# Kernel optimization log

Measured on AMD Instinct MI355X. Metric: run time of the kernel, lower is better.

Reference implementation:

```python
import jax, jax.numpy as jnp
import numpy as np

N_EXPERTS = 8
TOP_K = 2


def setup_inputs() -> dict:
    key = jax.random.key(0)
    ks = jax.random.split(key, 5)
    B, T, D, E, H = 4, 2048, 1024, N_EXPERTS, 2730  # H = int(2*D*4/3)
    x = jax.random.normal(ks[0], (B, T, D), dtype=jnp.float32)
    gate_w = jax.random.normal(ks[1], (E, D), dtype=jnp.float32) * 0.02
    w1 = jax.random.normal(ks[2], (E, H, D), dtype=jnp.float32) * 0.02
    w3 = jax.random.normal(ks[3], (E, H, D), dtype=jnp.float32) * 0.02
    w2 = jax.random.normal(ks[4], (E, D, H), dtype=jnp.float32) * 0.02
    return {"x": x, "gate_w": gate_w, "w1": w1, "w3": w3, "w2": w2}


def reference(x, gate_w, w1, w3, w2):
    B, T, D = x.shape
    E = gate_w.shape[0]
    x_flat = x.reshape(-1, D)  # [N, D], N = B*T
    N = x_flat.shape[0]

    # Router: top-k over softmax probabilities, renormalized over selected experts
    logits = x_flat @ gate_w.T                      # [N, E]
    probs = jax.nn.softmax(logits, axis=-1)         # [N, E]
    top_v, top_i = jax.lax.top_k(probs, TOP_K)      # [N, K]
    top_v = top_v / jnp.sum(top_v, axis=-1, keepdims=True)

    # Dense combine weights [N, E]: weight of expert e for each token (0 if not selected).
    # top_k indices are distinct per token, so scatter-add equals scatter-set here.
    combine = jnp.zeros((N, E), dtype=x.dtype).at[
        jnp.arange(N)[:, None], top_i
    ].add(top_v)

    # Weighted combine of SwiGLU experts (loop over small fixed expert count).
    out = jnp.zeros_like(x_flat)
    for e in range(E):
        gate = jax.nn.silu(x_flat @ w1[e].T)        # [N, H]
        up = x_flat @ w3[e].T                       # [N, H]
        y = (gate * up) @ w2[e].T                   # [N, D]
        out = out + combine[:, e:e + 1] * y

    aux_loss = jnp.asarray(0.0, dtype=x.dtype)  # use_aux_loss=False / eval mode
    return out.reshape(B, T, D), aux_loss
```

## Files before the change

### kernel.cpp

```cpp
#include <hip/hip_runtime.h>
#include <hip/hip_bf16.h>

#define N_TOK 8192
#define D_DIM 1024
#define E_NUM 8
#define H_DIM 2730
#define HP    2816
#define NP    5632
#define NROWS (N_TOK*2)
#define MAXTILES 136
#define MAXT256  72

typedef __bf16 bf16;
typedef __bf16 bf16x8 __attribute__((ext_vector_type(8)));
typedef __bf16 bf16x4 __attribute__((ext_vector_type(4)));
typedef float  f32x4  __attribute__((ext_vector_type(4)));

__device__ __forceinline__ void gload_lds16(const bf16* g, bf16* l) {
  __builtin_amdgcn_global_load_lds((const __attribute__((address_space(1))) void*)g,
                                   (__attribute__((address_space(3))) void*)l, 16, 0, 0);
}
#define VMCNT(n) asm volatile("s_waitcnt vmcnt(" #n ")" ::: "memory")
#define LGKM0()  asm volatile("s_waitcnt lgkmcnt(0)" ::: "memory")
#define BAR() __builtin_amdgcn_s_barrier()

__global__ void conv13_kernel(const float* __restrict__ w1, const float* __restrict__ w3,
                              bf16* __restrict__ Bp) {
  int i = blockIdx.x * blockDim.x + threadIdx.x;
  if (i >= E_NUM * NP * 128) return;
  int c8 = i & 127;
  int r  = (i >> 7) % NP;
  int e  = i / (NP * 128);
  int hc = ((r >> 5) << 4) + (r & 15);
  bf16x8 o;
  if (hc < H_DIM) {
    const float* s = (((r >> 4) & 1) ? w3 : w1) + ((long)e * H_DIM + hc) * D_DIM + c8 * 8;
    float4 a0 = ((const float4*)s)[0], a1 = ((const float4*)s)[1];
    o[0]=(bf16)a0.x; o[1]=(bf16)a0.y; o[2]=(bf16)a0.z; o[3]=(bf16)a0.w;
    o[4]=(bf16)a1.x; o[5]=(bf16)a1.y; o[6]=(bf16)a1.z; o[7]=(bf16)a1.w;
  } else {
    #pragma unroll
    for (int j = 0; j < 8; j++) o[j] = (bf16)0.f;
  }
  ((bf16x8*)Bp)[i] = o;
}

__global__ void conv_w2_kernel(const float* __restrict__ src, bf16* __restrict__ dst) {
  int i = blockIdx.x * blockDim.x + threadIdx.x;
  if (i >= E_NUM * D_DIM * (HP / 8)) return;
  int c8 = i % (HP / 8);
  int row = i / (HP / 8);
  int c = c8 * 8;
  const float* s = src + (long)row * H_DIM + c;
  bf16x8 o;
  #pragma unroll
  for (int j = 0; j < 8; j++) o[j] = (c + j < H_DIM) ? (bf16)s[j] : (bf16)0.f;
  ((bf16x8*)dst)[i] = o;
}

__global__ void router_kernel(const float* __restrict__ x, const float* __restrict__ gw,
                              int* __restrict__ topi, float* __restrict__ topw,
                              int* __restrict__ counts) {
  int t = blockIdx.x * (blockDim.x >> 6) + (threadIdx.x >> 6);
  int lane = threadIdx.x & 63;
  if (t >= N_TOK) return;
  const float* xr = x + (long)t * D_DIM;
  float acc[E_NUM];
  #pragma unroll
  for (int e = 0; e < E_NUM; e++) acc[e] = 0.f;
  for (int j = 0; j < D_DIM / 64; j++) {
    float xv = xr[j * 64 + lane];
    #pragma unroll
    for (int e = 0; e < E_NUM; e++) acc[e] += xv * gw[e * D_DIM + j * 64 + lane];
  }
  #pragma unroll
  for (int e = 0; e < E_NUM; e++) {
    float v = acc[e];
    #pragma unroll
    for (int s = 32; s > 0; s >>= 1) v += __shfl_xor(v, s, 64);
    acc[e] = v;
  }
  if (lane == 0) {
    int b0 = -1, b1 = -1; float v0 = -1e30f, v1 = -1e30f;
    #pragma unroll
    for (int e = 0; e < E_NUM; e++) {
      float v = acc[e];
      if (v > v0) { v1 = v0; b1 = b0; v0 = v; b0 = e; }
      else if (v > v1) { v1 = v; b1 = e; }
    }
    float w0 = 1.f / (1.f + expf(v1 - v0));
    topi[t * 2] = b0; topi[t * 2 + 1] = b1;
    topw[t * 2] = w0; topw[t * 2 + 1] = 1.f - w0;
    atomicAdd(&counts[b0], 1); atomicAdd(&counts[b1], 1);
  }
}

__global__ void tiles_kernel(const int* __restrict__ counts, int* __restrict__ offs,
                             int* __restrict__ tlist, int* __restrict__ tlist2) {
  if (threadIdx.x == 0) {
    int s = 0, idx = 0, idx2 = 0;
    for (int e = 0; e < E_NUM; e++) {
      offs[e] = s;
      int ne = counts[e];
      s += ne;
      int nt = (ne + 127) >> 7;
      for (int t = 0; t < nt; t++) tlist[idx++] = (e << 8) | t;
      int nt2 = (ne + 255) >> 8;
      for (int t = 0; t < nt2; t++) tlist2[idx2++] = (e << 8) | t;
    }
    offs[E_NUM] = s;
    for (; idx < MAXTILES; idx++) tlist[idx] = -1;
    for (; idx2 < MAXT256; idx2++) tlist2[idx2] = -1;
  }
}

__global__ void scatter_kernel(const int* __restrict__ topi, const float* __restrict__ topw,
                               const int* __restrict__ offs, int* __restrict__ cursor,
                               int* __restrict__ rowmap, float* __restrict__ roww,
                               int* __restrict__ rowoftok) {
  int i = blockIdx.x * blockDim.x + threadIdx.x;
  if (i >= NROWS) return;
  int e = topi[i];
  int pos = atomicAdd(&cursor[e], 1);
  int row = offs[e] + pos;
  rowmap[row] = i >> 1;
  roww[row] = topw[i];
  rowoftok[i] = row;
}

__global__ void gather_kernel(const float* __restrict__ x, const int* __restrict__ rowmap,
                              bf16* __restrict__ Xg) {
  int r = blockIdx.x * (blockDim.x >> 6) + (threadIdx.x >> 6);
  int lane = threadIdx.x & 63;
  if (r >= NROWS) return;
  int t = rowmap[r];
  const float4* src = (const float4*)(x + (long)t * D_DIM);
  bf16x4* dst = (bf16x4*)(Xg + (long)r * D_DIM);
  #pragma unroll
  for (int j = 0; j < 4; j++) {
    float4 v = src[j * 64 + lane];
    bf16x4 o; o[0]=(bf16)v.x; o[1]=(bf16)v.y; o[2]=(bf16)v.z; o[3]=(bf16)v.w;
    dst[j * 64 + lane] = o;
  }
}

__global__ void combine_kernel(const bf16* __restrict__ y, const int* __restrict__ rowoftok,
                               const float* __restrict__ topw, float* __restrict__ out) {
  int t = blockIdx.x * (blockDim.x >> 6) + (threadIdx.x >> 6);
  int lane = threadIdx.x & 63;
  if (t >= N_TOK) return;
  int r0 = rowoftok[t * 2], r1 = rowoftok[t * 2 + 1];
  float w0 = topw[t * 2], w1 = topw[t * 2 + 1];
  const bf16x8* y0 = (const bf16x8*)(y + (long)r0 * D_DIM);
  const bf16x8* y1 = (const bf16x8*)(y + (long)r1 * D_DIM);
  float* o = out + (long)t * D_DIM;
  #pragma unroll
  for (int j = 0; j < 2; j++) {
    bf16x8 a = y0[j * 64 + lane], b = y1[j * 64 + lane];
    float4 v0, v1;
    v0.x = w0*(float)a[0] + w1*(float)b[0]; v0.y = w0*(float)a[1] + w1*(float)b[1];
    v0.z = w0*(float)a[2] + w1*(float)b[2]; v0.w = w0*(float)a[3] + w1*(float)b[3];
    v1.x = w0*(float)a[4] + w1*(float)b[4]; v1.y = w0*(float)a[5] + w1*(float)b[5];
    v1.z = w0*(float)a[6] + w1*(float)b[6]; v1.w = w0*(float)a[7] + w1*(float)b[7];
    float4* op = (float4*)(o + (j * 64 + lane) * 8);
    op[0] = v0; op[1] = v1;
  }
}


#define G1_STAGE(T) do { int sb_ = ((T) & 3) * 8192; \
    gload_lds16(aSrc0 + (T) * 32, smem + sb_ + wv * 512); \
    gload_lds16(aSrc1 + (T) * 32, smem + sb_ + 4096 + wv * 512); \
    gload_lds16(bSrc0 + (T) * 32, smem + 32768 + sb_ + wv * 512); \
    gload_lds16(bSrc1 + (T) * 32, smem + 32768 + sb_ + 4096 + wv * 512); \
  } while (0)

#define G1_READ0(SB) do { \
    _Pragma("unroll") for (int m_ = 0; m_ < 4; m_++) \
      aF0[m_] = *(const bf16x8*)&smem[(SB) + (wr * 64 + m_ * 16 + fr) * 32 + qp]; \
    _Pragma("unroll") for (int q_ = 0; q_ < 4; q_++) \
      bF[q_] = *(const bf16x8*)&smem[32768 + (SB) + ((q_ >> 1) * 128 + wc * 32 + (q_ & 1) * 16 + fr) * 32 + qp]; \
  } while (0)

#define G1_MFMA0() do { __builtin_amdgcn_s_setprio(1); \
    _Pragma("unroll") for (int m_ = 0; m_ < 4; m_++) \
    _Pragma("unroll") for (int q_ = 0; q_ < 4; q_++) \
      acc[0][q_ >> 1][m_][q_ & 1] = __builtin_amdgcn_mfma_f32_16x16x32_bf16(aF0[m_], bF[q_], acc[0][q_ >> 1][m_][q_ & 1], 0, 0, 0); \
    __builtin_amdgcn_s_setprio(0); } while (0)

#define G1_READ1(SB) do { \
    _Pragma("unroll") for (int m_ = 0; m_ < 4; m_++) \
      aF1[m_] = *(const bf16x8*)&smem[(SB) + (128 + wr * 64 + m_ * 16 + fr) * 32 + qp]; \
  } while (0)

#define G1_MFMA1() do { __builtin_amdgcn_s_setprio(1); \
    _Pragma("unroll") for (int m_ = 0; m_ < 4; m_++) \
    _Pragma("unroll") for (int q_ = 0; q_ < 4; q_++) \
      acc[1][q_ >> 1][m_][q_ & 1] = __builtin_amdgcn_mfma_f32_16x16x32_bf16(aF1[m_], bF[q_], acc[1][q_ >> 1][m_][q_ & 1], 0, 0, 0); \
    __builtin_amdgcn_s_setprio(0); } while (0)

__global__ __launch_bounds__(512, 2) void gemm1_kernel(
    const bf16* __restrict__ Xg, const bf16* __restrict__ Bp,
    const int* __restrict__ counts, const int* __restrict__ offs,
    const int* __restrict__ tlist2, bf16* __restrict__ h) {
  int te = tlist2[blockIdx.x];
  if (te < 0) return;
  int e = te >> 8, tm = te & 255;
  int ne = counts[e];
  int row_base = offs[e];
  int n0 = blockIdx.y * 256;

  __shared__ bf16 smem[65536];
  int tid = threadIdx.x, wv = tid >> 6, lane = tid & 63;
  int wr = wv >> 2, wc = wv & 3;
  int fr = lane & 15, hi = lane >> 4;
  int qp = (hi ^ ((fr >> 1) & 3)) * 8;
  int srcq = ((lane & 3) ^ ((lane >> 3) & 3)) * 8;
  int srow = lane >> 2;

  f32x4 acc[2][2][4][2];
  #pragma unroll
  for (int a = 0; a < 2; a++)
    #pragma unroll
    for (int b = 0; b < 2; b++)
      #pragma unroll
      for (int m = 0; m < 4; m++)
        #pragma unroll
        for (int n = 0; n < 2; n++) acc[a][b][m][n] = (f32x4)0.f;

  const bf16* Bpe = Bp + (long)e * NP * D_DIM;
  int ra0 = row_base + min(tm * 256 + wv * 16 + srow, ne - 1);
  int ra1 = row_base + min(tm * 256 + 128 + wv * 16 + srow, ne - 1);
  const bf16* aSrc0 = Xg + (long)ra0 * D_DIM + srcq;
  const bf16* aSrc1 = Xg + (long)ra1 * D_DIM + srcq;
  const bf16* bSrc0 = Bpe + (long)(n0 + wv * 16 + srow) * D_DIM + srcq;
  const bf16* bSrc1 = Bpe + (long)(n0 + 128 + wv * 16 + srow) * D_DIM + srcq;

  bf16x8 aF0[4], aF1[4], bF[4];

  G1_STAGE(0); G1_STAGE(1); G1_STAGE(2);
  VMCNT(8); BAR();

  for (int t = 0; t < 29; t++) {
    int sb = (t & 3) * 8192;
    G1_READ0(sb);
    G1_STAGE(t + 3);
    BAR();
    G1_MFMA0();
    G1_READ1(sb);
    G1_MFMA1();
    LGKM0(); VMCNT(8); BAR();
  }
  { int sb = (29 & 3) * 8192; G1_READ0(sb); BAR(); G1_MFMA0(); G1_READ1(sb); G1_MFMA1(); LGKM0(); VMCNT(4); BAR(); }
  { int sb = (30 & 3) * 8192; G1_READ0(sb); BAR(); G1_MFMA0(); G1_READ1(sb); G1_MFMA1(); LGKM0(); VMCNT(0); BAR(); }
  { int sb = (31 & 3) * 8192; G1_READ0(sb); G1_MFMA0(); G1_READ1(sb); G1_MFMA1(); }

  int crow4 = hi * 4;
  #pragma unroll
  for (int mh = 0; mh < 2; mh++)
    #pragma unroll
    for (int m = 0; m < 4; m++)
      #pragma unroll
      for (int j = 0; j < 4; j++) {
        int rloc = tm * 256 + mh * 128 + wr * 64 + m * 16 + crow4 + j;
        if (rloc < ne) {
          long hrow = (long)(row_base + rloc) * HP;
          #pragma unroll
          for (int nh = 0; nh < 2; nh++) {
            int hc0 = (n0 + nh * 128 + wc * 32) >> 1;
            float g = acc[mh][nh][m][0][j], u = acc[mh][nh][m][1][j];
            h[hrow + hc0 + fr] = (bf16)((g / (1.f + __expf(-g))) * u);
          }
        }
      }
}

#define G2_STAGE(SB, T) do { \
    _Pragma("unroll") for (int L_ = 0; L_ < 2; L_++) \
      gload_lds16(aS[L_] + (T) * 32, smem2 + (SB) + w * 1024 + L_ * 512); \
    _Pragma("unroll") for (int L_ = 0; L_ < 4; L_++) \
      gload_lds16(bS[L_] + (T) * 32, smem2 + (SB) + 4096 + w * 2048 + L_ * 512); \
  } while (0)

#define G2_READ0(SB) do { \
    _Pragma("unroll") for (int m_ = 0; m_ < 4; m_++) \
      af[m_] = *(const bf16x8*)&smem2[(SB) + (wr * 64 + m_ * 16 + fr) * 32 + qp]; \
    _Pragma("unroll") for (int n_ = 0; n_ < 4; n_++) \
      bf0[n_] = *(const bf16x8*)&smem2[(SB) + 4096 + (wc * 128 + n_ * 16 + fr) * 32 + qp]; \
  } while (0)

#define G2_MFMA0() do { __builtin_amdgcn_s_setprio(1); \
    _Pragma("unroll") for (int m_ = 0; m_ < 4; m_++) \
    _Pragma("unroll") for (int n_ = 0; n_ < 4; n_++) \
      acc[m_][n_] = __builtin_amdgcn_mfma_f32_16x16x32_bf16(af[m_], bf0[n_], acc[m_][n_], 0, 0, 0); \
    __builtin_amdgcn_s_setprio(0); } while (0)

#define G2_READ1(SB) do { \
    _Pragma("unroll") for (int n_ = 0; n_ < 4; n_++) \
      bf1[n_] = *(const bf16x8*)&smem2[(SB) + 4096 + (wc * 128 + (n_ + 4) * 16 + fr) * 32 + qp]; \
  } while (0)

#define G2_MFMA1() do { __builtin_amdgcn_s_setprio(1); \
    _Pragma("unroll") for (int m_ = 0; m_ < 4; m_++) \
    _Pragma("unroll") for (int n_ = 0; n_ < 4; n_++) \
      acc[m_][n_ + 4] = __builtin_amdgcn_mfma_f32_16x16x32_bf16(af[m_], bf1[n_], acc[m_][n_ + 4], 0, 0, 0); \
    __builtin_amdgcn_s_setprio(0); } while (0)

__global__ __launch_bounds__(256, 2) void gemm2_kernel(
    const bf16* __restrict__ h, const bf16* __restrict__ w2b,
    const int* __restrict__ counts, const int* __restrict__ offs,
    const int* __restrict__ tlist, bf16* __restrict__ y) {
  int te = tlist[blockIdx.x];
  if (te < 0) return;
  int e = te >> 8, tm = te & 255;
  int ne = counts[e];
  int row_base = offs[e];
  int n0 = blockIdx.y * 256;

  __shared__ bf16 smem2[3 * 12288];
  int tid = threadIdx.x, w = tid >> 6, lane = tid & 63;
  int wr = w >> 1, wc = w & 1;
  int fr = lane & 15, hi = lane >> 4;
  int qp = (hi ^ ((fr >> 1) & 3)) * 8;
  int srcq = ((lane & 3) ^ ((lane >> 3) & 3)) * 8;
  int srow = lane >> 2;

  f32x4 acc[4][8];
  #pragma unroll
  for (int m = 0; m < 4; m++)
    #pragma unroll
    for (int n = 0; n < 8; n++) acc[m][n] = (f32x4)0.f;

  const bf16* w2e = w2b + (long)e * D_DIM * HP;
  const bf16* aS[2];
  const bf16* bS[4];
  #pragma unroll
  for (int L = 0; L < 2; L++) {
    int ra = row_base + min(tm * 128 + w * 32 + L * 16 + srow, ne - 1);
    aS[L] = h + (long)ra * HP + srcq;
  }
  #pragma unroll
  for (int L = 0; L < 4; L++) {
    int rb = n0 + w * 64 + L * 16 + srow;
    bS[L] = w2e + (long)rb * HP + srcq;
  }

  bf16x8 af[4], bf0[4], bf1[4];

  G2_STAGE(0, 0); G2_STAGE(12288, 1);
  VMCNT(6); BAR();

  int sbC = 0, sbS = 24576;
  for (int t = 0; t < 86; t++) {
    G2_READ0(sbC);
    G2_STAGE(sbS, t + 2);
    BAR();
    G2_MFMA0();
    G2_READ1(sbC);
    G2_MFMA1();
    LGKM0(); VMCNT(6); BAR();
    sbC += 12288; if (sbC > 24576) sbC = 0;
    sbS += 12288; if (sbS > 24576) sbS = 0;
  }
  { G2_READ0(sbC); BAR(); G2_MFMA0(); G2_READ1(sbC); G2_MFMA1(); LGKM0(); VMCNT(0); BAR();
    sbC += 12288; if (sbC > 24576) sbC = 0; }
  { G2_READ0(sbC); G2_MFMA0(); G2_READ1(sbC); G2_MFMA1(); }

  int crow4 = hi * 4;
  #pragma unroll
  for (int m = 0; m < 4; m++)
    #pragma unroll
    for (int j = 0; j < 4; j++) {
      int rloc = tm * 128 + wr * 64 + m * 16 + crow4 + j;
      if (rloc < ne) {
        long yrow = (long)(row_base + rloc) * D_DIM;
        #pragma unroll
        for (int n = 0; n < 8; n++) {
          int col = n0 + wc * 128 + n * 16 + fr;
          y[yrow + col] = (bf16)acc[m][n][j];
        }
      }
    }
}

extern "C" void kernel_launch(void* const* d_in, const int* in_sizes, int n_in,
                              void* d_out, int out_size, void* d_ws, size_t ws_size,
                              hipStream_t stream) {
  const float* x  = (const float*)d_in[0];
  const float* gw = (const float*)d_in[1];
  const float* w1 = (const float*)d_in[2];
  const float* w3 = (const float*)d_in[3];
  const float* w2 = (const float*)d_in[4];
  float* out = (float*)d_out;

  char* ws = (char*)d_ws;
  int*   counts   = (int*)(ws);
  int*   cursor   = (int*)(ws + 64);
  int*   offs     = (int*)(ws + 128);
  int*   tlist    = (int*)(ws + 192);
  int*   tlist2   = (int*)(ws + 768);
  int*   topi     = (int*)(ws + 2048);
  float* topw     = (float*)(ws + 2048 + 65536);
  int*   rowmap   = (int*)(ws + 2048 + 131072);
  float* roww     = (float*)(ws + 2048 + 196608);
  int*   rowoftok = (int*)(ws + 2048 + 262144);
  char*  big      = ws + 2048 + 327680;
  bf16* Bp   = (bf16*)big;
  bf16* w2b  = (bf16*)big;
  bf16* Xg   = Bp + (size_t)E_NUM * NP * D_DIM;
  bf16* hbuf = Xg + (size_t)NROWS * D_DIM;
  bf16* ybuf = Xg;

  hipMemsetAsync((char*)d_out + (size_t)(out_size - 1) * sizeof(float), 0, sizeof(float), stream);
  hipMemsetAsync(ws, 0, 256, stream);

  int nbp = E_NUM * NP * 128;
  conv13_kernel<<<(nbp + 255) / 256, 256, 0, stream>>>(w1, w3, Bp);

  router_kernel<<<N_TOK / 4, 256, 0, stream>>>(x, gw, topi, topw, counts);
  tiles_kernel<<<1, 64, 0, stream>>>(counts, offs, tlist, tlist2);
  scatter_kernel<<<(NROWS + 255) / 256, 256, 0, stream>>>(topi, topw, offs, cursor, rowmap, roww, rowoftok);
  gather_kernel<<<NROWS / 4, 256, 0, stream>>>(x, rowmap, Xg);

  dim3 g1(MAXT256, NP / 256);
  gemm1_kernel<<<g1, 512, 0, stream>>>(Xg, Bp, counts, offs, tlist2, hbuf);

  int w2n = E_NUM * D_DIM * (HP / 8);
  conv_w2_kernel<<<(w2n + 255) / 256, 256, 0, stream>>>(w2, w2b);

  dim3 g2(MAXTILES, D_DIM / 256);
  gemm2_kernel<<<g2, 256, 0, stream>>>(hbuf, w2b, counts, offs, tlist, ybuf);
  combine_kernel<<<N_TOK / 4, 256, 0, stream>>>(ybuf, rowoftok, topw, out);
}
```

Measured before the change: 758.9 us.

## Shrink GEMM1 to 128x256 tiles and GEMM2 to 128x128 tiles

GEMM1 drops its 256x256 tile and 512-thread block, 4-stage pipeline for a 128x256 tile with 256 threads and a 3-stage LDS ring, reusing the GEMM2 tile list. GEMM2 narrows its N tile from 256 to 128 and raises the occupancy hint to 3 blocks per CU. The aim is less per-expert padding waste and more blocks to fill the CUs. The cost is less operand reuse per block and more global traffic for the weight and activation reloads.

```diff
diff --git a/kernel.cpp b/kernel.cpp
--- a/kernel.cpp
+++ b/kernel.cpp
@@ -9,7 +9,6 @@
 #define NP    5632
 #define NROWS (N_TOK*2)
 #define MAXTILES 136
-#define MAXT256  72
 
 typedef __bf16 bf16;
 typedef __bf16 bf16x8 __attribute__((ext_vector_type(8)));
@@ -96,21 +95,18 @@
 }
 
 __global__ void tiles_kernel(const int* __restrict__ counts, int* __restrict__ offs,
-                             int* __restrict__ tlist, int* __restrict__ tlist2) {
+                             int* __restrict__ tlist) {
   if (threadIdx.x == 0) {
-    int s = 0, idx = 0, idx2 = 0;
+    int s = 0, idx = 0;
     for (int e = 0; e < E_NUM; e++) {
       offs[e] = s;
       int ne = counts[e];
       s += ne;
       int nt = (ne + 127) >> 7;
       for (int t = 0; t < nt; t++) tlist[idx++] = (e << 8) | t;
-      int nt2 = (ne + 255) >> 8;
-      for (int t = 0; t < nt2; t++) tlist2[idx2++] = (e << 8) | t;
     }
     offs[E_NUM] = s;
     for (; idx < MAXTILES; idx++) tlist[idx] = -1;
-    for (; idx2 < MAXT256; idx2++) tlist2[idx2] = -1;
   }
 }
 
@@ -168,145 +164,136 @@
 }
 
 
-#define G1_STAGE(T) do { int sb_ = ((T) & 3) * 8192; \
-    gload_lds16(aSrc0 + (T) * 32, smem + sb_ + wv * 512); \
-    gload_lds16(aSrc1 + (T) * 32, smem + sb_ + 4096 + wv * 512); \
-    gload_lds16(bSrc0 + (T) * 32, smem + 32768 + sb_ + wv * 512); \
-    gload_lds16(bSrc1 + (T) * 32, smem + 32768 + sb_ + 4096 + wv * 512); \
+#define G1_STAGE(SB, T) do { \
+    _Pragma("unroll") for (int L_ = 0; L_ < 2; L_++) \
+      gload_lds16(aS[L_] + (T) * 32, smem + (SB) + w * 1024 + L_ * 512); \
+    _Pragma("unroll") for (int L_ = 0; L_ < 4; L_++) \
+      gload_lds16(bS[L_] + (T) * 32, smem + (SB) + 4096 + w * 2048 + L_ * 512); \
   } while (0)
 
 #define G1_READ0(SB) do { \
     _Pragma("unroll") for (int m_ = 0; m_ < 4; m_++) \
-      aF0[m_] = *(const bf16x8*)&smem[(SB) + (wr * 64 + m_ * 16 + fr) * 32 + qp]; \
+      af[m_] = *(const bf16x8*)&smem[(SB) + (wr * 64 + m_ * 16 + fr) * 32 + qp]; \
     _Pragma("unroll") for (int q_ = 0; q_ < 4; q_++) \
-      bF[q_] = *(const bf16x8*)&smem[32768 + (SB) + ((q_ >> 1) * 128 + wc * 32 + (q_ & 1) * 16 + fr) * 32 + qp]; \
+      bf0[q_] = *(const bf16x8*)&smem[(SB) + 4096 + (wc * 128 + q_ * 16 + fr) * 32 + qp]; \
   } while (0)
 
 #define G1_MFMA0() do { __builtin_amdgcn_s_setprio(1); \
     _Pragma("unroll") for (int m_ = 0; m_ < 4; m_++) \
     _Pragma("unroll") for (int q_ = 0; q_ < 4; q_++) \
-      acc[0][q_ >> 1][m_][q_ & 1] = __builtin_amdgcn_mfma_f32_16x16x32_bf16(aF0[m_], bF[q_], acc[0][q_ >> 1][m_][q_ & 1], 0, 0, 0); \
+      acc[m_][q_] = __builtin_amdgcn_mfma_f32_16x16x32_bf16(af[m_], bf0[q_], acc[m_][q_], 0, 0, 0); \
     __builtin_amdgcn_s_setprio(0); } while (0)
 
 #define G1_READ1(SB) do { \
-    _Pragma("unroll") for (int m_ = 0; m_ < 4; m_++) \
-      aF1[m_] = *(const bf16x8*)&smem[(SB) + (128 + wr * 64 + m_ * 16 + fr) * 32 + qp]; \
+    _Pragma("unroll") for (int q_ = 0; q_ < 4; q_++) \
+      bf1[q_] = *(const bf16x8*)&smem[(SB) + 4096 + (wc * 128 + (q_ + 4) * 16 + fr) * 32 + qp]; \
   } while (0)
 
 #define G1_MFMA1() do { __builtin_amdgcn_s_setprio(1); \
     _Pragma("unroll") for (int m_ = 0; m_ < 4; m_++) \
     _Pragma("unroll") for (int q_ = 0; q_ < 4; q_++) \
-      acc[1][q_ >> 1][m_][q_ & 1] = __builtin_amdgcn_mfma_f32_16x16x32_bf16(aF1[m_], bF[q_], acc[1][q_ >> 1][m_][q_ & 1], 0, 0, 0); \
+      acc[m_][q_ + 4] = __builtin_amdgcn_mfma_f32_16x16x32_bf16(af[m_], bf1[q_], acc[m_][q_ + 4], 0, 0, 0); \
     __builtin_amdgcn_s_setprio(0); } while (0)
 
-__global__ __launch_bounds__(512, 2) void gemm1_kernel(
+__global__ __launch_bounds__(256, 2) void gemm1_kernel(
     const bf16* __restrict__ Xg, const bf16* __restrict__ Bp,
     const int* __restrict__ counts, const int* __restrict__ offs,
-    const int* __restrict__ tlist2, bf16* __restrict__ h) {
-  int te = tlist2[blockIdx.x];
+    const int* __restrict__ tlist, bf16* __restrict__ h) {
+  int te = tlist[blockIdx.x];
   if (te < 0) return;
   int e = te >> 8, tm = te & 255;
   int ne = counts[e];
   int row_base = offs[e];
   int n0 = blockIdx.y * 256;
 
-  __shared__ bf16 smem[65536];
-  int tid = threadIdx.x, wv = tid >> 6, lane = tid & 63;
-  int wr = wv >> 2, wc = wv & 3;
+  __shared__ bf16 smem[3 * 12288];
+  int tid = threadIdx.x, w = tid >> 6, lane = tid & 63;
+  int wr = w >> 1, wc = w & 1;
   int fr = lane & 15, hi = lane >> 4;
   int qp = (hi ^ ((fr >> 1) & 3)) * 8;
   int srcq = ((lane & 3) ^ ((lane >> 3) & 3)) * 8;
   int srow = lane >> 2;
 
-  f32x4 acc[2][2][4][2];
-  #pragma unroll
-  for (int a = 0; a < 2; a++)
-    #pragma unroll
-    for (int b = 0; b < 2; b++)
-      #pragma unroll
-      for (int m = 0; m < 4; m++)
-        #pragma unroll
-        for (int n = 0; n < 2; n++) acc[a][b][m][n] = (f32x4)0.f;
+  f32x4 acc[4][8];
+  #pragma unroll
+  for (int m = 0; m < 4; m++)
+    #pragma unroll
+    for (int q = 0; q < 8; q++) acc[m][q] = (f32x4)0.f;
 
   const bf16* Bpe = Bp + (long)e * NP * D_DIM;
-  int ra0 = row_base + min(tm * 256 + wv * 16 + srow, ne - 1);
-  int ra1 = row_base + min(tm * 256 + 128 + wv * 16 + srow, ne - 1);
-  const bf16* aSrc0 = Xg + (long)ra0 * D_DIM + srcq;
-  const bf16* aSrc1 = Xg + (long)ra1 * D_DIM + srcq;
-  const bf16* bSrc0 = Bpe + (long)(n0 + wv * 16 + srow) * D_DIM + srcq;
-  const bf16* bSrc1 = Bpe + (long)(n0 + 128 + wv * 16 + srow) * D_DIM + srcq;
-
-  bf16x8 aF0[4], aF1[4], bF[4];
-
-  G1_STAGE(0); G1_STAGE(1); G1_STAGE(2);
-  VMCNT(8); BAR();
-
-  for (int t = 0; t < 29; t++) {
-    int sb = (t & 3) * 8192;
-    G1_READ0(sb);
-    G1_STAGE(t + 3);
+  const bf16* aS[2];
+  const bf16* bS[4];
+  #pragma unroll
+  for (int L = 0; L < 2; L++) {
+    int ra = row_base + min(tm * 128 + w * 32 + L * 16 + srow, ne - 1);
+    aS[L] = Xg + (long)ra * D_DIM + srcq;
+  }
+  #pragma unroll
+  for (int L = 0; L < 4; L++) {
+    int rb = n0 + w * 64 + L * 16 + srow;
+    bS[L] = Bpe + (long)rb * D_DIM + srcq;
+  }
+
+  bf16x8 af[4], bf0[4], bf1[4];
+
+  G1_STAGE(0, 0); G1_STAGE(12288, 1);
+  VMCNT(6); BAR();
+
+  int sbC = 0, sbS = 24576;
+  for (int t = 0; t < 30; t++) {
+    G1_READ0(sbC);
+    G1_STAGE(sbS, t + 2);
     BAR();
     G1_MFMA0();
-    G1_READ1(sb);
+    G1_READ1(sbC);
     G1_MFMA1();
-    LGKM0(); VMCNT(8); BAR();
-  }
-  { int sb = (29 & 3) * 8192; G1_READ0(sb); BAR(); G1_MFMA0(); G1_READ1(sb); G1_MFMA1(); LGKM0(); VMCNT(4); BAR(); }
-  { int sb = (30 & 3) * 8192; G1_READ0(sb); BAR(); G1_MFMA0(); G1_READ1(sb); G1_MFMA1(); LGKM0(); VMCNT(0); BAR(); }
-  { int sb = (31 & 3) * 8192; G1_READ0(sb); G1_MFMA0(); G1_READ1(sb); G1_MFMA1(); }
+    LGKM0(); VMCNT(6); BAR();
+    sbC += 12288; if (sbC > 24576) sbC = 0;
+    sbS += 12288; if (sbS > 24576) sbS = 0;
+  }
+  { G1_READ0(sbC); BAR(); G1_MFMA0(); G1_READ1(sbC); G1_MFMA1(); LGKM0(); VMCNT(0); BAR();
+    sbC += 12288; if (sbC > 24576) sbC = 0; }
+  { G1_READ0(sbC); G1_MFMA0(); G1_READ1(sbC); G1_MFMA1(); }
 
   int crow4 = hi * 4;
   #pragma unroll
-  for (int mh = 0; mh < 2; mh++)
-    #pragma unroll
-    for (int m = 0; m < 4; m++)
-      #pragma unroll
-      for (int j = 0; j < 4; j++) {
-        int rloc = tm * 256 + mh * 128 + wr * 64 + m * 16 + crow4 + j;
-        if (rloc < ne) {
-          long hrow = (long)(row_base + rloc) * HP;
-          #pragma unroll
-          for (int nh = 0; nh < 2; nh++) {
-            int hc0 = (n0 + nh * 128 + wc * 32) >> 1;
-            float g = acc[mh][nh][m][0][j], u = acc[mh][nh][m][1][j];
-            h[hrow + hc0 + fr] = (bf16)((g / (1.f + __expf(-g))) * u);
-          }
+  for (int m = 0; m < 4; m++)
+    #pragma unroll
+    for (int j = 0; j < 4; j++) {
+      int rloc = tm * 128 + wr * 64 + m * 16 + crow4 + j;
+      if (rloc < ne) {
+        long hrow = (long)(row_base + rloc) * HP;
+        #pragma unroll
+        for (int p = 0; p < 4; p++) {
+          int col = (n0 >> 1) + wc * 64 + p * 16 + fr;
+          float g = acc[m][2 * p][j], u = acc[m][2 * p + 1][j];
+          h[hrow + col] = (bf16)((g / (1.f + __expf(-g))) * u);
         }
       }
+    }
 }
 
 #define G2_STAGE(SB, T) do { \
     _Pragma("unroll") for (int L_ = 0; L_ < 2; L_++) \
       gload_lds16(aS[L_] + (T) * 32, smem2 + (SB) + w * 1024 + L_ * 512); \
-    _Pragma("unroll") for (int L_ = 0; L_ < 4; L_++) \
-      gload_lds16(bS[L_] + (T) * 32, smem2 + (SB) + 4096 + w * 2048 + L_ * 512); \
+    _Pragma("unroll") for (int L_ = 0; L_ < 2; L_++) \
+      gload_lds16(bS[L_] + (T) * 32, smem2 + (SB) + 4096 + w * 1024 + L_ * 512); \
   } while (0)
 
-#define G2_READ0(SB) do { \
+#define G2_READ(SB) do { \
     _Pragma("unroll") for (int m_ = 0; m_ < 4; m_++) \
       af[m_] = *(const bf16x8*)&smem2[(SB) + (wr * 64 + m_ * 16 + fr) * 32 + qp]; \
     _Pragma("unroll") for (int n_ = 0; n_ < 4; n_++) \
-      bf0[n_] = *(const bf16x8*)&smem2[(SB) + 4096 + (wc * 128 + n_ * 16 + fr) * 32 + qp]; \
+      bfr[n_] = *(const bf16x8*)&smem2[(SB) + 4096 + (wc * 64 + n_ * 16 + fr) * 32 + qp]; \
   } while (0)
 
-#define G2_MFMA0() do { __builtin_amdgcn_s_setprio(1); \
+#define G2_MFMA() do { __builtin_amdgcn_s_setprio(1); \
     _Pragma("unroll") for (int m_ = 0; m_ < 4; m_++) \
     _Pragma("unroll") for (int n_ = 0; n_ < 4; n_++) \
-      acc[m_][n_] = __builtin_amdgcn_mfma_f32_16x16x32_bf16(af[m_], bf0[n_], acc[m_][n_], 0, 0, 0); \
+      acc[m_][n_] = __builtin_amdgcn_mfma_f32_16x16x32_bf16(af[m_], bfr[n_], acc[m_][n_], 0, 0, 0); \
     __builtin_amdgcn_s_setprio(0); } while (0)
 
-#define G2_READ1(SB) do { \
-    _Pragma("unroll") for (int n_ = 0; n_ < 4; n_++) \
-      bf1[n_] = *(const bf16x8*)&smem2[(SB) + 4096 + (wc * 128 + (n_ + 4) * 16 + fr) * 32 + qp]; \
-  } while (0)
-
-#define G2_MFMA1() do { __builtin_amdgcn_s_setprio(1); \
-    _Pragma("unroll") for (int m_ = 0; m_ < 4; m_++) \
-    _Pragma("unroll") for (int n_ = 0; n_ < 4; n_++) \
-      acc[m_][n_ + 4] = __builtin_amdgcn_mfma_f32_16x16x32_bf16(af[m_], bf1[n_], acc[m_][n_ + 4], 0, 0, 0); \
-    __builtin_amdgcn_s_setprio(0); } while (0)
-
-__global__ __launch_bounds__(256, 2) void gemm2_kernel(
+__global__ __launch_bounds__(256, 3) void gemm2_kernel(
     const bf16* __restrict__ h, const bf16* __restrict__ w2b,
     const int* __restrict__ counts, const int* __restrict__ offs,
     const int* __restrict__ tlist, bf16* __restrict__ y) {
@@ -315,9 +302,9 @@
   int e = te >> 8, tm = te & 255;
   int ne = counts[e];
   int row_base = offs[e];
-  int n0 = blockIdx.y * 256;
-
-  __shared__ bf16 smem2[3 * 12288];
+  int n0 = blockIdx.y * 128;
+
+  __shared__ bf16 smem2[3 * 8192];
   int tid = threadIdx.x, w = tid >> 6, lane = tid & 63;
   int wr = w >> 1, wc = w & 1;
   int fr = lane & 15, hi = lane >> 4;
@@ -325,46 +312,41 @@
   int srcq = ((lane & 3) ^ ((lane >> 3) & 3)) * 8;
   int srow = lane >> 2;
 
-  f32x4 acc[4][8];
+  f32x4 acc[4][4];
   #pragma unroll
   for (int m = 0; m < 4; m++)
     #pragma unroll
-    for (int n = 0; n < 8; n++) acc[m][n] = (f32x4)0.f;
+    for (int n = 0; n < 4; n++) acc[m][n] = (f32x4)0.f;
 
   const bf16* w2e = w2b + (long)e * D_DIM * HP;
   const bf16* aS[2];
-  const bf16* bS[4];
+  const bf16* bS[2];
   #pragma unroll
   for (int L = 0; L < 2; L++) {
     int ra = row_base + min(tm * 128 + w * 32 + L * 16 + srow, ne - 1);
     aS[L] = h + (long)ra * HP + srcq;
-  }
-  #pragma unroll
-  for (int L = 0; L < 4; L++) {
-    int rb = n0 + w * 64 + L * 16 + srow;
+    int rb = n0 + w * 32 + L * 16 + srow;
     bS[L] = w2e + (long)rb * HP + srcq;
   }
 
-  bf16x8 af[4], bf0[4], bf1[4];
-
-  G2_STAGE(0, 0); G2_STAGE(12288, 1);
-  VMCNT(6); BAR();
-
-  int sbC = 0, sbS = 24576;
+  bf16x8 af[4], bfr[4];
+
+  G2_STAGE(0, 0); G2_STAGE(8192, 1);
+  VMCNT(4); BAR();
+
+  int sbC = 0, sbS = 16384;
   for (int t = 0; t < 86; t++) {
-    G2_READ0(sbC);
+    G2_READ(sbC);
     G2_STAGE(sbS, t + 2);
     BAR();
-    G2_MFMA0();
-    G2_READ1(sbC);
-    G2_MFMA1();
-    LGKM0(); VMCNT(6); BAR();
-    sbC += 12288; if (sbC > 24576) sbC = 0;
-    sbS += 12288; if (sbS > 24576) sbS = 0;
-  }
-  { G2_READ0(sbC); BAR(); G2_MFMA0(); G2_READ1(sbC); G2_MFMA1(); LGKM0(); VMCNT(0); BAR();
-    sbC += 12288; if (sbC > 24576) sbC = 0; }
-  { G2_READ0(sbC); G2_MFMA0(); G2_READ1(sbC); G2_MFMA1(); }
+    G2_MFMA();
+    LGKM0(); VMCNT(4); BAR();
+    sbC += 8192; if (sbC > 16384) sbC = 0;
+    sbS += 8192; if (sbS > 16384) sbS = 0;
+  }
+  { G2_READ(sbC); BAR(); G2_MFMA(); LGKM0(); VMCNT(0); BAR();
+    sbC += 8192; if (sbC > 16384) sbC = 0; }
+  { G2_READ(sbC); G2_MFMA(); }
 
   int crow4 = hi * 4;
   #pragma unroll
@@ -375,8 +357,8 @@
       if (rloc < ne) {
         long yrow = (long)(row_base + rloc) * D_DIM;
         #pragma unroll
-        for (int n = 0; n < 8; n++) {
-          int col = n0 + wc * 128 + n * 16 + fr;
+        for (int n = 0; n < 4; n++) {
+          int col = n0 + wc * 64 + n * 16 + fr;
           y[yrow + col] = (bf16)acc[m][n][j];
         }
       }
@@ -398,7 +380,6 @@
   int*   cursor   = (int*)(ws + 64);
   int*   offs     = (int*)(ws + 128);
   int*   tlist    = (int*)(ws + 192);
-  int*   tlist2   = (int*)(ws + 768);
   int*   topi     = (int*)(ws + 2048);
   float* topw     = (float*)(ws + 2048 + 65536);
   int*   rowmap   = (int*)(ws + 2048 + 131072);
@@ -418,17 +399,17 @@
   conv13_kernel<<<(nbp + 255) / 256, 256, 0, stream>>>(w1, w3, Bp);
 
   router_kernel<<<N_TOK / 4, 256, 0, stream>>>(x, gw, topi, topw, counts);
-  tiles_kernel<<<1, 64, 0, stream>>>(counts, offs, tlist, tlist2);
+  tiles_kernel<<<1, 64, 0, stream>>>(counts, offs, tlist);
   scatter_kernel<<<(NROWS + 255) / 256, 256, 0, stream>>>(topi, topw, offs, cursor, rowmap, roww, rowoftok);
   gather_kernel<<<NROWS / 4, 256, 0, stream>>>(x, rowmap, Xg);
 
-  dim3 g1(MAXT256, NP / 256);
-  gemm1_kernel<<<g1, 512, 0, stream>>>(Xg, Bp, counts, offs, tlist2, hbuf);
+  dim3 g1(MAXTILES, NP / 256);
+  gemm1_kernel<<<g1, 256, 0, stream>>>(Xg, Bp, counts, offs, tlist, hbuf);
 
   int w2n = E_NUM * D_DIM * (HP / 8);
   conv_w2_kernel<<<(w2n + 255) / 256, 256, 0, stream>>>(w2, w2b);
 
-  dim3 g2(MAXTILES, D_DIM / 256);
+  dim3 g2(MAXTILES, D_DIM / 128);
   gemm2_kernel<<<g2, 256, 0, stream>>>(hbuf, w2b, counts, offs, tlist, ybuf);
   combine_kernel<<<N_TOK / 4, 256, 0, stream>>>(ybuf, rowoftok, topw, out);
 }
```

Result: no change. 755.6 us (-0.4%).
